# Performance work log

Hardware: AMD Instinct MI355X
Metric: run time of the kernel (lower is better)

The kernel has to match this reference:

```python
import jax, jax.numpy as jnp
import numpy as np

CELL_SIDE = 0.5
GRID_N = 6
HIDDEN = 128


def setup_inputs() -> dict:
    key = jax.random.key(0)
    k1, k2, k3 = jax.random.split(key, 3)
    N = 8192
    obs = jax.random.normal(k1, (N, 2), dtype=jnp.float32)          # agent (x, y) positions
    W = jax.random.normal(k2, (HIDDEN, GRID_N * GRID_N), dtype=jnp.float32) * 0.1  # Linear weight
    b = jax.random.normal(k3, (HIDDEN,), dtype=jnp.float32) * 0.1   # Linear bias
    return {"obs": obs, "W": W, "b": b}


def reference(obs, W, b):
    # Vectorized equivalent of per-agent occupancy + Linear embedding.
    N = obs.shape[0]
    g = GRID_N
    # relative grid coordinates of agent j w.r.t. agent i: [N, N, 2]
    rel = (obs[None, :, :] - obs[:, None, :]) / CELL_SIDE + g / 2.0
    # validity: both coords in [0, g), j != i, neither position is NaN
    in_range = jnp.all((rel >= 0) & (rel < g), axis=-1)             # [N, N]
    not_self = ~jnp.eye(N, dtype=bool)
    valid = ~jnp.isnan(obs[:, 0])                                   # [N]
    w = (in_range & not_self & valid[None, :] & valid[:, None]).astype(obs.dtype)
    # integer cell indices (floor == trunc since valid rel >= 0); clip keeps masked-out
    # (weight 0) entries in-bounds for the scatter.
    ij = jnp.floor(rel).astype(jnp.int32)
    cell = jnp.clip(ij[..., 0], 0, g - 1) * g + jnp.clip(ij[..., 1], 0, g - 1)  # [N, N]
    flat_idx = (jnp.arange(N, dtype=jnp.int32)[:, None] * (g * g) + cell).reshape(-1)
    occ = jnp.zeros((N * g * g,), obs.dtype).at[flat_idx].add(w.reshape(-1))
    occ = occ.reshape(N, g * g)                                     # [N, 36]
    return occ @ W.T + b                                            # [N, 128]
```

## Files before the change

### kernel.cpp

```cpp
#include <hip/hip_runtime.h>

#define NAGENT 8192
#define NCELL 36
#define HIDDEN 128

__global__ __launch_bounds__(256) void occ_hist_kernel(
    const float2* __restrict__ obs, unsigned* __restrict__ occ) {
  __shared__ unsigned cnt[64 * NCELL];
  const int tid = threadIdx.x;
  for (int k = tid; k < 64 * NCELL; k += 256) cnt[k] = 0u;
  __syncthreads();

  const int ag   = blockIdx.x >> 3;
  const int jq   = blockIdx.x & 7;
  const int lane = tid & 63;
  const int wv   = tid >> 6;
  const int agent = ag * 64 + lane;

  const float2 oi = obs[agent];
  const float xi = oi.x, yi = oi.y;

  unsigned* myCnt = &cnt[lane * NCELL];

  const int jbeg = jq * 1024 + wv * 256;
  const int jend = jbeg + 256;
#pragma unroll 4
  for (int j = jbeg; j < jend; ++j) {
    const float2 oj = obs[j];
    const float rx = (oj.x - xi) * 2.0f + 3.0f;
    const float ry = (oj.y - yi) * 2.0f + 3.0f;
    if (rx >= 0.0f && rx < 6.0f && ry >= 0.0f && ry < 6.0f) {
      const int cell = (int)rx * 6 + (int)ry;
      atomicAdd(&myCnt[cell], 1u);
    }
  }
  __syncthreads();

  unsigned* gbase = occ + (size_t)ag * 64 * NCELL;
  for (int k = tid; k < 64 * NCELL; k += 256) {
    const unsigned v = cnt[k];
    if (v) atomicAdd(&gbase[k], v);
  }
}

__global__ __launch_bounds__(256) void occ_gemm_kernel(
    const unsigned* __restrict__ occ, const float* __restrict__ W,
    const float* __restrict__ bias, float* __restrict__ out) {
  __shared__ float Wl[HIDDEN * NCELL];
  const int tid = threadIdx.x;
  for (int k = tid; k < HIDDEN * NCELL; k += 256) Wl[k] = W[k];
  __syncthreads();

  const int a  = blockIdx.x * 16 + (tid >> 4);
  const int hg = tid & 15;

  const uint4* occ4 = (const uint4*)(occ + (size_t)a * NCELL);
  float occf[NCELL];
#pragma unroll
  for (int q = 0; q < 9; ++q) {
    const uint4 v = occ4[q];
    occf[4 * q + 0] = (float)v.x;
    occf[4 * q + 1] = (float)v.y;
    occf[4 * q + 2] = (float)v.z;
    occf[4 * q + 3] = (float)v.w;
  }
  occf[21] -= 1.0f;

  float acc[8];
#pragma unroll
  for (int k = 0; k < 8; ++k) acc[k] = bias[hg + 16 * k];

#pragma unroll
  for (int c4 = 0; c4 < 9; ++c4) {
#pragma unroll
    for (int k = 0; k < 8; ++k) {
      const float4 w4 = *(const float4*)&Wl[(hg + 16 * k) * NCELL + c4 * 4];
      acc[k] = fmaf(occf[4 * c4 + 0], w4.x, acc[k]);
      acc[k] = fmaf(occf[4 * c4 + 1], w4.y, acc[k]);
      acc[k] = fmaf(occf[4 * c4 + 2], w4.z, acc[k]);
      acc[k] = fmaf(occf[4 * c4 + 3], w4.w, acc[k]);
    }
  }

  float* ob = out + (size_t)a * HIDDEN;
#pragma unroll
  for (int k = 0; k < 8; ++k) ob[hg + 16 * k] = acc[k];
}

extern "C" void kernel_launch(void* const* d_in, const int* in_sizes, int n_in,
                              void* d_out, int out_size, void* d_ws, size_t ws_size,
                              hipStream_t stream) {
  (void)in_sizes; (void)n_in; (void)out_size; (void)ws_size;
  const float2* obs = (const float2*)d_in[0];
  const float*  W   = (const float*)d_in[1];
  const float*  b   = (const float*)d_in[2];
  float* out = (float*)d_out;
  unsigned* occ = (unsigned*)d_ws;

  hipMemsetAsync(occ, 0, (size_t)NAGENT * NCELL * sizeof(unsigned), stream);

  occ_hist_kernel<<<dim3(1024), dim3(256), 0, stream>>>(obs, occ);
  occ_gemm_kernel<<<dim3(512), dim3(256), 0, stream>>>(occ, W, b, out);
}
```

Measured before the change: 103.4 us.

## Replace global atomics and memset with packed per-chunk partial histograms

Each block now writes its own partial histogram slice, with two 16-bit counts packed per word, so the memset and the global atomic merge are no longer needed. The GEMM kernel sums the partials across chunks and removes the self count there. The change also pads the shared histogram stride to 37 to cut LDS bank conflicts and loads two agents per float4. The chunk count depends on workspace size, which can change the grid and the parallelism, and the 16-bit packing assumes no cell count exceeds 65535 within a chunk.

```diff
diff --git a/kernel.cpp b/kernel.cpp
--- a/kernel.cpp
+++ b/kernel.cpp
@@ -3,68 +3,87 @@
 #define NAGENT 8192
 #define NCELL 36
 #define HIDDEN 128
+#define CSTRIDE 37
+#define PWORDS 18
 
 __global__ __launch_bounds__(256) void occ_hist_kernel(
-    const float2* __restrict__ obs, unsigned* __restrict__ occ) {
-  __shared__ unsigned cnt[64 * NCELL];
+    const float2* __restrict__ obs, unsigned* __restrict__ partial, int jrange) {
+  __shared__ unsigned cnt[64 * CSTRIDE];
   const int tid = threadIdx.x;
-  for (int k = tid; k < 64 * NCELL; k += 256) cnt[k] = 0u;
+  for (int k = tid; k < 64 * CSTRIDE; k += 256) cnt[k] = 0u;
   __syncthreads();
 
-  const int ag   = blockIdx.x >> 3;
-  const int jq   = blockIdx.x & 7;
   const int lane = tid & 63;
   const int wv   = tid >> 6;
-  const int agent = ag * 64 + lane;
+  const int agent = blockIdx.y * 64 + lane;
 
   const float2 oi = obs[agent];
   const float xi = oi.x, yi = oi.y;
+  unsigned* myCnt = &cnt[lane * CSTRIDE];
 
-  unsigned* myCnt = &cnt[lane * NCELL];
+  const int jbeg = blockIdx.x * jrange + wv * (jrange >> 2);
+  const float4* jp = (const float4*)obs + (jbeg >> 1);
+  const int nIter = jrange >> 3;
 
-  const int jbeg = jq * 1024 + wv * 256;
-  const int jend = jbeg + 256;
 #pragma unroll 4
-  for (int j = jbeg; j < jend; ++j) {
-    const float2 oj = obs[j];
-    const float rx = (oj.x - xi) * 2.0f + 3.0f;
-    const float ry = (oj.y - yi) * 2.0f + 3.0f;
-    if (rx >= 0.0f && rx < 6.0f && ry >= 0.0f && ry < 6.0f) {
-      const int cell = (int)rx * 6 + (int)ry;
-      atomicAdd(&myCnt[cell], 1u);
+  for (int t = 0; t < nIter; ++t) {
+    const float4 o2 = jp[t];
+    {
+      const float rx = fmaf(o2.x - xi, 2.0f, 3.0f);
+      const float ry = fmaf(o2.y - yi, 2.0f, 3.0f);
+      if (rx >= 0.0f && rx < 6.0f && ry >= 0.0f && ry < 6.0f)
+        atomicAdd(&myCnt[(int)rx * 6 + (int)ry], 1u);
+    }
+    {
+      const float rx = fmaf(o2.z - xi, 2.0f, 3.0f);
+      const float ry = fmaf(o2.w - yi, 2.0f, 3.0f);
+      if (rx >= 0.0f && rx < 6.0f && ry >= 0.0f && ry < 6.0f)
+        atomicAdd(&myCnt[(int)rx * 6 + (int)ry], 1u);
     }
   }
   __syncthreads();
 
-  unsigned* gbase = occ + (size_t)ag * 64 * NCELL;
-  for (int k = tid; k < 64 * NCELL; k += 256) {
-    const unsigned v = cnt[k];
-    if (v) atomicAdd(&gbase[k], v);
+  unsigned* gbase = partial +
+      ((size_t)blockIdx.x * NAGENT + (size_t)blockIdx.y * 64) * PWORDS;
+  for (int k = tid; k < 64 * PWORDS; k += 256) {
+    const int a = k / PWORDS, w = k - a * PWORDS;
+    const unsigned lo = cnt[a * CSTRIDE + 2 * w];
+    const unsigned hi = cnt[a * CSTRIDE + 2 * w + 1];
+    gbase[k] = lo | (hi << 16);
   }
 }
 
 __global__ __launch_bounds__(256) void occ_gemm_kernel(
-    const unsigned* __restrict__ occ, const float* __restrict__ W,
-    const float* __restrict__ bias, float* __restrict__ out) {
+    const unsigned* __restrict__ partial, const float* __restrict__ W,
+    const float* __restrict__ bias, float* __restrict__ out, int nchunk) {
   __shared__ float Wl[HIDDEN * NCELL];
+  __shared__ float occ[16 * CSTRIDE];
   const int tid = threadIdx.x;
-  for (int k = tid; k < HIDDEN * NCELL; k += 256) Wl[k] = W[k];
+
+  const float4* W4 = (const float4*)W;
+  float4* Wl4 = (float4*)Wl;
+  for (int k = tid; k < HIDDEN * NCELL / 4; k += 256) Wl4[k] = W4[k];
+
+  const int agBase = blockIdx.x * 16;
+  for (int k = tid; k < 16 * PWORDS; k += 256) {
+    const int a = k / PWORDS, w = k - a * PWORDS;
+    const unsigned* p = partial + (size_t)(agBase + a) * PWORDS + w;
+    unsigned s = 0;
+    for (int c = 0; c < nchunk; ++c) s += p[(size_t)c * NAGENT * PWORDS];
+    float lo = (float)(s & 0xFFFFu);
+    float hi = (float)(s >> 16);
+    if (w == 10) hi = fmaxf(hi - 1.0f, 0.0f);
+    occ[a * CSTRIDE + 2 * w]     = lo;
+    occ[a * CSTRIDE + 2 * w + 1] = hi;
+  }
   __syncthreads();
 
-  const int a  = blockIdx.x * 16 + (tid >> 4);
+  const int a  = tid >> 4;
   const int hg = tid & 15;
 
-  const uint4* occ4 = (const uint4*)(occ + (size_t)a * NCELL);
   float occf[NCELL];
 #pragma unroll
-  for (int q = 0; q < 9; ++q) {
-    const uint4 v = occ4[q];
-    occf[4 * q + 0] = (float)v.x;
-    occf[4 * q + 1] = (float)v.y;
-    occf[4 * q + 2] = (float)v.z;
-    occf[4 * q + 3] = (float)v.w;
-  }
-  occf[21] -= 1.0f;
+  for (int c = 0; c < NCELL; ++c) occf[c] = occ[a * CSTRIDE + c];
 
   float acc[8];
 #pragma unroll
@@ -82,7 +101,7 @@
     }
   }
 
-  float* ob = out + (size_t)a * HIDDEN;
+  float* ob = out + (size_t)(agBase + a) * HIDDEN;
 #pragma unroll
   for (int k = 0; k < 8; ++k) ob[hg + 16 * k] = acc[k];
 }
@@ -90,15 +109,19 @@
 extern "C" void kernel_launch(void* const* d_in, const int* in_sizes, int n_in,
                               void* d_out, int out_size, void* d_ws, size_t ws_size,
                               hipStream_t stream) {
-  (void)in_sizes; (void)n_in; (void)out_size; (void)ws_size;
+  (void)in_sizes; (void)n_in; (void)out_size;
   const float2* obs = (const float2*)d_in[0];
   const float*  W   = (const float*)d_in[1];
   const float*  b   = (const float*)d_in[2];
   float* out = (float*)d_out;
-  unsigned* occ = (unsigned*)d_ws;
+  unsigned* partial = (unsigned*)d_ws;
 
-  hipMemsetAsync(occ, 0, (size_t)NAGENT * NCELL * sizeof(unsigned), stream);
+  int nchunk = 2;
+  for (int c = 16; c >= 2; c >>= 1) {
+    if (ws_size >= (size_t)c * NAGENT * PWORDS * sizeof(unsigned)) { nchunk = c; break; }
+  }
+  const int jrange = NAGENT / nchunk;
 
-  occ_hist_kernel<<<dim3(1024), dim3(256), 0, stream>>>(obs, occ);
-  occ_gemm_kernel<<<dim3(512), dim3(256), 0, stream>>>(occ, W, b, out);
+  occ_hist_kernel<<<dim3(nchunk, 128), dim3(256), 0, stream>>>(obs, partial, jrange);
+  occ_gemm_kernel<<<dim3(512), dim3(256), 0, stream>>>(partial, W, b, out, nchunk);
 }
```

Result: faster. 98.38 us (-4.8%).
